# Optimization experiments

Hardware: AMD Instinct MI355X
Metric: run time of the kernel (lower is better)

## Reference

```python
import jax, jax.numpy as jnp
import numpy as np

N_SCALES = 3
BASE_SIGMA = 0.1
SCALES = jnp.asarray([BASE_SIGMA * 2.0 ** i for i in range(N_SCALES)], dtype=jnp.float32)


def setup_inputs() -> dict:
    key = jax.random.key(0)
    k_x, k_pos, k_tp, k_w1, k_b1, k_w2, k_b2 = jax.random.split(key, 7)
    B, C, T = 16, 306, 4000
    M = 128
    x = jax.random.normal(k_x, (B, C, T), dtype=jnp.float32)
    positions = jax.random.normal(k_pos, (B, C, 2), dtype=jnp.float32)
    target_positions = jax.random.normal(k_tp, (M, 2), dtype=jnp.float32)
    # nn.Linear(3, 32) / nn.Linear(32, 1) params (kaiming-uniform-ish init)
    lim1 = 1.0 / np.sqrt(3.0)
    w1 = jax.random.uniform(k_w1, (3, 32), jnp.float32, -lim1, lim1)
    b1 = jax.random.uniform(k_b1, (32,), jnp.float32, -lim1, lim1)
    lim2 = 1.0 / np.sqrt(32.0)
    w2 = jax.random.uniform(k_w2, (32, 1), jnp.float32, -lim2, lim2)
    b2 = jax.random.uniform(k_b2, (1,), jnp.float32, -lim2, lim2)
    return {"x": x, "positions": positions, "target_positions": target_positions,
            "w1": w1, "b1": b1, "w2": w2, "b2": b2}


def reference(x, positions, target_positions, w1, b1, w2, b2):
    # squared euclidean distances [B, C, M]
    diff = positions[:, :, None, :] - target_positions[None, None, :, :]
    d2 = jnp.sum(diff * diff, axis=-1)
    # multi-scale Gaussian kernels, stacked on last axis -> [B, C, M, n_scales]
    inv = 1.0 / (2.0 * SCALES ** 2)  # [n_scales]
    scale_weights = jnp.exp(-d2[..., None] * inv)
    # tiny 2-layer MLP gate: (3 -> 32 -> 1)
    h = jax.nn.relu(scale_weights @ w1 + b1)  # [B, C, M, 32]
    w = (h @ w2 + b2)[..., 0]                 # [B, C, M]
    # normalize over channel dim
    w = w / (jnp.sum(w, axis=1, keepdims=True) + 1e-8)
    # weighted channel aggregation -> [B, M, T]
    return jnp.einsum('bct,bcm->bmt', x, w)
```

## Files before the change

kernel.cpp:

```cpp
#include <hip/hip_runtime.h>

#define B_ 16
#define C_ 306
#define CP_ 320
#define T_ 4000
#define M_ 128

typedef short bf16x8 __attribute__((ext_vector_type(8)));
typedef float f32x4 __attribute__((ext_vector_type(4)));

__global__ __launch_bounds__(320)
void gate_kernel(const float* __restrict__ positions,
                 const float* __restrict__ target,
                 const float* __restrict__ w1,
                 const float* __restrict__ b1,
                 const float* __restrict__ w2,
                 const float* __restrict__ b2,
                 unsigned short* __restrict__ w_hi,
                 unsigned short* __restrict__ w_lo,
                 float* __restrict__ scale) {
    const int b  = blockIdx.x >> 5;
    const int mg = blockIdx.x & 31;
    const int tid = threadIdx.x;

    __shared__ float s_w1[96], s_b1[32], s_w2[32];
    __shared__ float2 s_pos[C_];
    __shared__ float s_b2;
    __shared__ float s_tgt[8];
    __shared__ float s_part[5];

    if (tid < 96) s_w1[tid] = w1[tid];
    if (tid < 32) { s_b1[tid] = b1[tid]; s_w2[tid] = w2[tid]; }
    if (tid == 256) s_b2 = b2[0];
    if (tid < C_) s_pos[tid] = ((const float2*)positions)[b * C_ + tid];
    if (tid >= 312) s_tgt[tid - 312] = target[mg * 8 + (tid - 312)];
    __syncthreads();

    float px = 0.0f, py = 0.0f;
    if (tid < C_) { px = s_pos[tid].x; py = s_pos[tid].y; }

#pragma unroll
    for (int mi = 0; mi < 4; ++mi) {
        float w = 0.0f;
        if (tid < C_) {
            const float dx = px - s_tgt[mi * 2 + 0];
            const float dy = py - s_tgt[mi * 2 + 1];
            const float d2 = dx * dx + dy * dy;
            const float s2 = __expf(-d2 * 3.125f);
            const float q  = s2 * s2;
            const float s1 = q * q;
            const float r  = s1 * s1;
            const float s0 = r * r;
            float acc = s_b2;
#pragma unroll
            for (int j = 0; j < 32; ++j) {
                float h = fmaf(s0, s_w1[j],
                          fmaf(s1, s_w1[32 + j],
                          fmaf(s2, s_w1[64 + j], s_b1[j])));
                acc = fmaf(fmaxf(h, 0.0f), s_w2[j], acc);
            }
            w = acc;
        }

        float s = w;
#pragma unroll
        for (int off = 32; off > 0; off >>= 1) s += __shfl_down(s, off, 64);
        if ((tid & 63) == 0) s_part[tid >> 6] = s;
        __syncthreads();
        if (tid == 0) {
            float tot = s_part[0] + s_part[1] + s_part[2] + s_part[3] + s_part[4];
            scale[b * M_ + mg * 4 + mi] = 1.0f / (tot + 1e-8f);
        }
        __syncthreads();

        const unsigned int u = __float_as_uint(w);
        const unsigned short h = (unsigned short)(u >> 16);
        const float lof = w - __uint_as_float(u & 0xffff0000u);
        const unsigned short l = (unsigned short)(__float_as_uint(lof) >> 16);
        const size_t off = (size_t)(b * M_ + mg * 4 + mi) * CP_ + tid;
        w_hi[off] = h;
        w_lo[off] = l;
    }
}

__global__ __launch_bounds__(256, 3)
void merge_gemm(const float* __restrict__ x,
                const unsigned short* __restrict__ w_hi,
                const unsigned short* __restrict__ w_lo,
                const float* __restrict__ scale,
                float* __restrict__ out) {
    const int t0 = blockIdx.x * 128;
    const int b  = blockIdx.y;
    const int tid  = threadIdx.x;
    const int lane = tid & 63;
    const int wv   = tid >> 6;
    const int tquad = lane >> 4;
    const int tsub  = lane & 15;

    __shared__ __align__(16) unsigned short sXh[8192];
    __shared__ __align__(16) unsigned short sXl[8192];
    __shared__ __align__(16) float sScale[M_];

    if (tid < M_) sScale[tid] = scale[b * M_ + tid];

    const float* xb = x + (size_t)b * C_ * T_;
    const unsigned short* whB = w_hi + (size_t)b * M_ * CP_;
    const unsigned short* wlB = w_lo + (size_t)b * M_ * CP_;

    f32x4 acc[4][4];
#pragma unroll
    for (int i = 0; i < 4; ++i)
#pragma unroll
        for (int j = 0; j < 4; ++j) acc[i][j] = (f32x4){0.f, 0.f, 0.f, 0.f};

    const int mw = (wv & 1) * 64;
    const int tw = (wv >> 1) * 64;

    for (int step = 0; step < CP_ / 64; ++step) {
        const int c0 = step * 64;

#pragma unroll
        for (int s = 0; s < 2; ++s) {
            const int t = wv * 16 + tsub + s * 64;
            const int tg = min(t0 + t, T_ - 1);
            const float* xcol = xb + tg;
#pragma unroll
            for (int k = 0; k < 8; ++k) {
                const int p = tquad + 4 * k;
                const int c = c0 + 2 * p;
                const int ca = min(c, C_ - 1);
                const int cb = min(c + 1, C_ - 1);
                const float xa = xcol[(size_t)ca * T_];
                const float xv = xcol[(size_t)cb * T_];
                const unsigned int ua = __float_as_uint(xa);
                const unsigned int ub = __float_as_uint(xv);
                const unsigned int hp = (ua >> 16) | (ub & 0xffff0000u);
                const float la = xa - __uint_as_float(ua & 0xffff0000u);
                const float lb = xv - __uint_as_float(ub & 0xffff0000u);
                const unsigned int lp = (__float_as_uint(la) >> 16) |
                                        (__float_as_uint(lb) & 0xffff0000u);
                const int off32 = (p >> 2) * 512 + t * 4 + (p & 3);
                ((unsigned int*)sXh)[off32] = hp;
                ((unsigned int*)sXl)[off32] = lp;
            }
        }
        __syncthreads();

#pragma unroll
        for (int ks = 0; ks < 2; ++ks) {
            const int cb0 = c0 + ks * 32;

            bf16x8 bh[4], bl[4];
#pragma unroll
            for (int i = 0; i < 4; ++i) {
                const int toff = ((ks * 4 + tquad) * 128 + tw + i * 16 + tsub) * 8;
                bh[i] = *(const bf16x8*)(sXh + toff);
                bl[i] = *(const bf16x8*)(sXl + toff);
            }
#pragma unroll
            for (int mi = 0; mi < 4; ++mi) {
                const size_t woff = (size_t)(mw + mi * 16 + tsub) * CP_ + cb0 + tquad * 8;
                const bf16x8 ah = *(const bf16x8*)(whB + woff);
                const bf16x8 al = *(const bf16x8*)(wlB + woff);
#pragma unroll
                for (int ti = 0; ti < 4; ++ti) {
                    acc[mi][ti] = __builtin_amdgcn_mfma_f32_16x16x32_bf16(
                        ah, bh[ti], acc[mi][ti], 0, 0, 0);
                    acc[mi][ti] = __builtin_amdgcn_mfma_f32_16x16x32_bf16(
                        ah, bl[ti], acc[mi][ti], 0, 0, 0);
                    acc[mi][ti] = __builtin_amdgcn_mfma_f32_16x16x32_bf16(
                        al, bh[ti], acc[mi][ti], 0, 0, 0);
                }
            }
        }
        __syncthreads();
    }

#pragma unroll
    for (int mi = 0; mi < 4; ++mi) {
        const int mbase = mw + mi * 16 + tquad * 4;
        const float4 sc = *(const float4*)(sScale + mbase);
#pragma unroll
        for (int ti = 0; ti < 4; ++ti) {
            const int tg = t0 + tw + ti * 16 + tsub;
            if (tg < T_) {
                float* op = out + ((size_t)b * M_ + mbase) * T_ + tg;
                op[0 * T_] = acc[mi][ti][0] * sc.x;
                op[1 * T_] = acc[mi][ti][1] * sc.y;
                op[2 * T_] = acc[mi][ti][2] * sc.z;
                op[3 * T_] = acc[mi][ti][3] * sc.w;
            }
        }
    }
}

extern "C" void kernel_launch(void* const* d_in, const int* in_sizes, int n_in,
                              void* d_out, int out_size, void* d_ws, size_t ws_size,
                              hipStream_t stream) {
    const float* x         = (const float*)d_in[0];
    const float* positions = (const float*)d_in[1];
    const float* target    = (const float*)d_in[2];
    const float* w1        = (const float*)d_in[3];
    const float* b1        = (const float*)d_in[4];
    const float* w2        = (const float*)d_in[5];
    const float* b2        = (const float*)d_in[6];
    float* out = (float*)d_out;

    unsigned short* w_hi = (unsigned short*)d_ws;
    unsigned short* w_lo = w_hi + (size_t)B_ * M_ * CP_;
    float* scale = (float*)(w_lo + (size_t)B_ * M_ * CP_);

    gate_kernel<<<B_ * 32, 320, 0, stream>>>(positions, target, w1, b1, w2, b2,
                                             w_hi, w_lo, scale);

    dim3 grid((T_ + 127) / 128, B_);
    merge_gemm<<<grid, 256, 0, stream>>>(x, w_hi, w_lo, scale, out);
}
```

Baseline: 151.4 us.

## Shrink GEMM tiles to 64x64, add M split, vectorize and prefetch x loads

The merge GEMM now uses 64(M)x64(T) tiles with a grid that also splits M, which gives more blocks for better CU occupancy. The x tile is loaded as float4 along T into registers and prefetched one step ahead, so the global load latency overlaps with the MFMA work. The padded LDS layout is meant to reduce bank conflicts. The trade-off is that x is now read twice, once per M half, and the smaller tiles give less reuse per block.

```diff
diff --git a/kernel.cpp b/kernel.cpp
--- a/kernel.cpp
+++ b/kernel.cpp
@@ -83,87 +83,110 @@
     }
 }
 
-__global__ __launch_bounds__(256, 3)
+__global__ __launch_bounds__(256, 4)
 void merge_gemm(const float* __restrict__ x,
                 const unsigned short* __restrict__ w_hi,
                 const unsigned short* __restrict__ w_lo,
                 const float* __restrict__ scale,
                 float* __restrict__ out) {
-    const int t0 = blockIdx.x * 128;
-    const int b  = blockIdx.y;
+    const int t0 = blockIdx.x * 64;
+    const int m0 = blockIdx.y * 64;
+    const int b  = blockIdx.z;
     const int tid  = threadIdx.x;
     const int lane = tid & 63;
     const int wv   = tid >> 6;
     const int tquad = lane >> 4;
     const int tsub  = lane & 15;
 
-    __shared__ __align__(16) unsigned short sXh[8192];
-    __shared__ __align__(16) unsigned short sXl[8192];
-    __shared__ __align__(16) float sScale[M_];
-
-    if (tid < M_) sScale[tid] = scale[b * M_ + tid];
+    __shared__ __align__(16) unsigned int sXh[2076];
+    __shared__ __align__(16) unsigned int sXl[2076];
+    __shared__ __align__(16) float sScale[64];
+
+    if (tid < 64) sScale[tid] = scale[b * M_ + m0 + tid];
 
     const float* xb = x + (size_t)b * C_ * T_;
-    const unsigned short* whB = w_hi + (size_t)b * M_ * CP_;
-    const unsigned short* wlB = w_lo + (size_t)b * M_ * CP_;
-
-    f32x4 acc[4][4];
-#pragma unroll
-    for (int i = 0; i < 4; ++i)
-#pragma unroll
-        for (int j = 0; j < 4; ++j) acc[i][j] = (f32x4){0.f, 0.f, 0.f, 0.f};
-
-    const int mw = (wv & 1) * 64;
-    const int tw = (wv >> 1) * 64;
-
-    for (int step = 0; step < CP_ / 64; ++step) {
-        const int c0 = step * 64;
-
-#pragma unroll
-        for (int s = 0; s < 2; ++s) {
-            const int t = wv * 16 + tsub + s * 64;
-            const int tg = min(t0 + t, T_ - 1);
-            const float* xcol = xb + tg;
-#pragma unroll
-            for (int k = 0; k < 8; ++k) {
-                const int p = tquad + 4 * k;
-                const int c = c0 + 2 * p;
-                const int ca = min(c, C_ - 1);
-                const int cb = min(c + 1, C_ - 1);
-                const float xa = xcol[(size_t)ca * T_];
-                const float xv = xcol[(size_t)cb * T_];
-                const unsigned int ua = __float_as_uint(xa);
-                const unsigned int ub = __float_as_uint(xv);
-                const unsigned int hp = (ua >> 16) | (ub & 0xffff0000u);
-                const float la = xa - __uint_as_float(ua & 0xffff0000u);
-                const float lb = xv - __uint_as_float(ub & 0xffff0000u);
-                const unsigned int lp = (__float_as_uint(la) >> 16) |
-                                        (__float_as_uint(lb) & 0xffff0000u);
-                const int off32 = (p >> 2) * 512 + t * 4 + (p & 3);
-                ((unsigned int*)sXh)[off32] = hp;
-                ((unsigned int*)sXl)[off32] = lp;
-            }
-        }
-        __syncthreads();
-
+    const unsigned short* whB = w_hi + (size_t)(b * M_ + m0) * CP_;
+    const unsigned short* wlB = w_lo + (size_t)(b * M_ + m0) * CP_;
+
+    const int mw = (wv & 1) * 32;
+    const int tw = (wv >> 1) * 32;
+
+    const int pp   = tid >> 4;
+    const int tq   = tid & 15;
+    const int runw = pp >> 1;
+    const int w0   = (pp & 1) * 2;
+    const float* xcol = xb + min(t0 + tq * 4, T_ - 4);
+
+    f32x4 acc[2][2];
+#pragma unroll
+    for (int i = 0; i < 2; ++i)
+#pragma unroll
+        for (int j = 0; j < 2; ++j) acc[i][j] = (f32x4){0.f, 0.f, 0.f, 0.f};
+
+    float4 rv[4];
+#pragma unroll
+    for (int r = 0; r < 4; ++r) {
+        const int c = min(pp * 4 + r, C_ - 1);
+        rv[r] = *(const float4*)(xcol + (size_t)c * T_);
+    }
+
+    for (int step = 0; step < 5; ++step) {
+        __syncthreads();
+        {
+            const float* f0 = (const float*)&rv[0];
+            const float* f1 = (const float*)&rv[1];
+            const float* f2 = (const float*)&rv[2];
+            const float* f3 = (const float*)&rv[3];
+            const int base = runw * 260 + tq * 16 + w0;
+#pragma unroll
+            for (int j = 0; j < 4; ++j) {
+                const unsigned int u0 = __float_as_uint(f0[j]);
+                const unsigned int u1 = __float_as_uint(f1[j]);
+                const unsigned int u2 = __float_as_uint(f2[j]);
+                const unsigned int u3 = __float_as_uint(f3[j]);
+                const unsigned int h01 = (u0 >> 16) | (u1 & 0xffff0000u);
+                const unsigned int h23 = (u2 >> 16) | (u3 & 0xffff0000u);
+                const float l0 = f0[j] - __uint_as_float(u0 & 0xffff0000u);
+                const float l1 = f1[j] - __uint_as_float(u1 & 0xffff0000u);
+                const float l2 = f2[j] - __uint_as_float(u2 & 0xffff0000u);
+                const float l3 = f3[j] - __uint_as_float(u3 & 0xffff0000u);
+                const unsigned int l01 = (__float_as_uint(l0) >> 16) |
+                                         (__float_as_uint(l1) & 0xffff0000u);
+                const unsigned int l23 = (__float_as_uint(l2) >> 16) |
+                                         (__float_as_uint(l3) & 0xffff0000u);
+                *(uint2*)(sXh + base + j * 4) = make_uint2(h01, h23);
+                *(uint2*)(sXl + base + j * 4) = make_uint2(l01, l23);
+            }
+        }
+        __syncthreads();
+
+        if (step < 4) {
+            const int c0n = (step + 1) * 64;
+#pragma unroll
+            for (int r = 0; r < 4; ++r) {
+                const int c = min(c0n + pp * 4 + r, C_ - 1);
+                rv[r] = *(const float4*)(xcol + (size_t)c * T_);
+            }
+        }
+
+        const int cbase = step * 64;
 #pragma unroll
         for (int ks = 0; ks < 2; ++ks) {
-            const int cb0 = c0 + ks * 32;
-
-            bf16x8 bh[4], bl[4];
-#pragma unroll
-            for (int i = 0; i < 4; ++i) {
-                const int toff = ((ks * 4 + tquad) * 128 + tw + i * 16 + tsub) * 8;
-                bh[i] = *(const bf16x8*)(sXh + toff);
-                bl[i] = *(const bf16x8*)(sXl + toff);
-            }
-#pragma unroll
-            for (int mi = 0; mi < 4; ++mi) {
-                const size_t woff = (size_t)(mw + mi * 16 + tsub) * CP_ + cb0 + tquad * 8;
+            bf16x8 bh[2], bl[2];
+#pragma unroll
+            for (int i = 0; i < 2; ++i) {
+                const int a = (ks * 4 + tquad) * 260 + (tw + i * 16 + tsub) * 4;
+                bh[i] = *(const bf16x8*)(sXh + a);
+                bl[i] = *(const bf16x8*)(sXl + a);
+            }
+#pragma unroll
+            for (int mi = 0; mi < 2; ++mi) {
+                const size_t woff = (size_t)(mw + mi * 16 + tsub) * CP_
+                                  + cbase + ks * 32 + tquad * 8;
                 const bf16x8 ah = *(const bf16x8*)(whB + woff);
                 const bf16x8 al = *(const bf16x8*)(wlB + woff);
 #pragma unroll
-                for (int ti = 0; ti < 4; ++ti) {
+                for (int ti = 0; ti < 2; ++ti) {
                     acc[mi][ti] = __builtin_amdgcn_mfma_f32_16x16x32_bf16(
                         ah, bh[ti], acc[mi][ti], 0, 0, 0);
                     acc[mi][ti] = __builtin_amdgcn_mfma_f32_16x16x32_bf16(
@@ -173,22 +196,21 @@
                 }
             }
         }
-        __syncthreads();
-    }
-
-#pragma unroll
-    for (int mi = 0; mi < 4; ++mi) {
-        const int mbase = mw + mi * 16 + tquad * 4;
-        const float4 sc = *(const float4*)(sScale + mbase);
-#pragma unroll
-        for (int ti = 0; ti < 4; ++ti) {
+    }
+
+#pragma unroll
+    for (int mi = 0; mi < 2; ++mi) {
+        const int mloc = mw + mi * 16 + tquad * 4;
+        const float4 sc = *(const float4*)(sScale + mloc);
+        float* op = out + ((size_t)b * M_ + m0 + mloc) * T_;
+#pragma unroll
+        for (int ti = 0; ti < 2; ++ti) {
             const int tg = t0 + tw + ti * 16 + tsub;
             if (tg < T_) {
-                float* op = out + ((size_t)b * M_ + mbase) * T_ + tg;
-                op[0 * T_] = acc[mi][ti][0] * sc.x;
-                op[1 * T_] = acc[mi][ti][1] * sc.y;
-                op[2 * T_] = acc[mi][ti][2] * sc.z;
-                op[3 * T_] = acc[mi][ti][3] * sc.w;
+                op[(size_t)0 * T_ + tg] = acc[mi][ti][0] * sc.x;
+                op[(size_t)1 * T_ + tg] = acc[mi][ti][1] * sc.y;
+                op[(size_t)2 * T_ + tg] = acc[mi][ti][2] * sc.z;
+                op[(size_t)3 * T_ + tg] = acc[mi][ti][3] * sc.w;
             }
         }
     }
@@ -213,6 +235,6 @@
     gate_kernel<<<B_ * 32, 320, 0, stream>>>(positions, target, w1, b1, w2, b2,
                                              w_hi, w_lo, scale);
 
-    dim3 grid((T_ + 127) / 128, B_);
+    dim3 grid((T_ + 63) / 64, 2, B_);
     merge_gemm<<<grid, 256, 0, stream>>>(x, w_hi, w_lo, scale, out);
 }
```

Measured after the change: 174.2 us. 1.15x slower.

## Vectorize x loads with register prefetch and fragment-ordered gate weights

Applied to the files above, without the earlier changes.

The GEMM now loads x as float4 along T into registers one K-step ahead, so global loads overlap the MFMA work, and writes them into a padded LDS layout that avoids bank conflicts. The gate kernel stages its hi/lo bf16 weights in shared memory and writes them to global memory in MFMA-fragment order, interleaving hi and lo, so the GEMM reads each A fragment pair contiguously. This removes the scalar strided x loads and the separate scattered hi/lo weight reads, at the cost of more registers for the prefetch buffers and a more complex indexing scheme.

```diff
diff --git a/kernel.cpp b/kernel.cpp
--- a/kernel.cpp
+++ b/kernel.cpp
@@ -8,6 +8,8 @@
 
 typedef short bf16x8 __attribute__((ext_vector_type(8)));
 typedef float f32x4 __attribute__((ext_vector_type(4)));
+
+#define WF_PER_B 81920
 
 __global__ __launch_bounds__(320)
 void gate_kernel(const float* __restrict__ positions,
@@ -16,8 +18,7 @@
                  const float* __restrict__ b1,
                  const float* __restrict__ w2,
                  const float* __restrict__ b2,
-                 unsigned short* __restrict__ w_hi,
-                 unsigned short* __restrict__ w_lo,
+                 unsigned short* __restrict__ wf,
                  float* __restrict__ scale) {
     const int b  = blockIdx.x >> 5;
     const int mg = blockIdx.x & 31;
@@ -28,6 +29,7 @@
     __shared__ float s_b2;
     __shared__ float s_tgt[8];
     __shared__ float s_part[5];
+    __shared__ unsigned short s_frag[40 * 72];
 
     if (tid < 96) s_w1[tid] = w1[tid];
     if (tid < 32) { s_b1[tid] = b1[tid]; s_w2[tid] = w2[tid]; }
@@ -38,6 +40,9 @@
 
     float px = 0.0f, py = 0.0f;
     if (tid < C_) { px = s_pos[tid].x; py = s_pos[tid].y; }
+
+    const int chunk = tid >> 3;
+    const int slot  = tid & 7;
 
 #pragma unroll
     for (int mi = 0; mi < 4; ++mi) {
@@ -77,16 +82,24 @@
         const unsigned short h = (unsigned short)(u >> 16);
         const float lof = w - __uint_as_float(u & 0xffff0000u);
         const unsigned short l = (unsigned short)(__float_as_uint(lof) >> 16);
-        const size_t off = (size_t)(b * M_ + mg * 4 + mi) * CP_ + tid;
-        w_hi[off] = h;
-        w_lo[off] = l;
+        s_frag[chunk * 72 + mi * 16 + 0 + slot] = h;
+        s_frag[chunk * 72 + mi * 16 + 8 + slot] = l;
+    }
+    __syncthreads();
+
+    {
+        const int ch = tid >> 3;
+        const int g  = tid & 7;
+        const uint4 v = *(const uint4*)(s_frag + ch * 72 + g * 8);
+        unsigned short* dst = wf + (size_t)b * WF_PER_B
+                            + (size_t)ch * 2048 + mg * 64 + g * 8;
+        *(uint4*)dst = v;
     }
 }
 
 __global__ __launch_bounds__(256, 3)
 void merge_gemm(const float* __restrict__ x,
-                const unsigned short* __restrict__ w_hi,
-                const unsigned short* __restrict__ w_lo,
+                const unsigned short* __restrict__ wf,
                 const float* __restrict__ scale,
                 float* __restrict__ out) {
     const int t0 = blockIdx.x * 128;
@@ -97,15 +110,14 @@
     const int tquad = lane >> 4;
     const int tsub  = lane & 15;
 
-    __shared__ __align__(16) unsigned short sXh[8192];
-    __shared__ __align__(16) unsigned short sXl[8192];
+    __shared__ __align__(16) unsigned int sXh[5120];
+    __shared__ __align__(16) unsigned int sXl[5120];
     __shared__ __align__(16) float sScale[M_];
 
     if (tid < M_) sScale[tid] = scale[b * M_ + tid];
 
     const float* xb = x + (size_t)b * C_ * T_;
-    const unsigned short* whB = w_hi + (size_t)b * M_ * CP_;
-    const unsigned short* wlB = w_lo + (size_t)b * M_ * CP_;
+    const unsigned short* wfB = wf + (size_t)b * WF_PER_B;
 
     f32x4 acc[4][4];
 #pragma unroll
@@ -116,52 +128,89 @@
     const int mw = (wv & 1) * 64;
     const int tw = (wv >> 1) * 64;
 
-    for (int step = 0; step < CP_ / 64; ++step) {
-        const int c0 = step * 64;
+    const int p  = tid >> 4;
+    const int tq = tid & 15;
+
+    float4 rv[8];
+#pragma unroll
+    for (int s = 0; s < 2; ++s) {
+        const int TQ  = tq + 16 * s;
+        const int tcl = min(t0 + TQ * 4, T_ - 4);
+#pragma unroll
+        for (int sub = 0; sub < 2; ++sub) {
+            const int cp = p + 16 * sub;
+            const int c  = 2 * cp;
+            rv[(s * 2 + sub) * 2 + 0] =
+                *(const float4*)(xb + (size_t)min(c, C_ - 1) * T_ + tcl);
+            rv[(s * 2 + sub) * 2 + 1] =
+                *(const float4*)(xb + (size_t)min(c + 1, C_ - 1) * T_ + tcl);
+        }
+    }
+
+    for (int step = 0; step < 5; ++step) {
+        __syncthreads();
 
 #pragma unroll
         for (int s = 0; s < 2; ++s) {
-            const int t = wv * 16 + tsub + s * 64;
-            const int tg = min(t0 + t, T_ - 1);
-            const float* xcol = xb + tg;
-#pragma unroll
-            for (int k = 0; k < 8; ++k) {
-                const int p = tquad + 4 * k;
-                const int c = c0 + 2 * p;
-                const int ca = min(c, C_ - 1);
-                const int cb = min(c + 1, C_ - 1);
-                const float xa = xcol[(size_t)ca * T_];
-                const float xv = xcol[(size_t)cb * T_];
-                const unsigned int ua = __float_as_uint(xa);
-                const unsigned int ub = __float_as_uint(xv);
-                const unsigned int hp = (ua >> 16) | (ub & 0xffff0000u);
-                const float la = xa - __uint_as_float(ua & 0xffff0000u);
-                const float lb = xv - __uint_as_float(ub & 0xffff0000u);
-                const unsigned int lp = (__float_as_uint(la) >> 16) |
-                                        (__float_as_uint(lb) & 0xffff0000u);
-                const int off32 = (p >> 2) * 512 + t * 4 + (p & 3);
-                ((unsigned int*)sXh)[off32] = hp;
-                ((unsigned int*)sXl)[off32] = lp;
-            }
-        }
-        __syncthreads();
+            const int TQ = tq + 16 * s;
+#pragma unroll
+            for (int sub = 0; sub < 2; ++sub) {
+                const int cp  = p + 16 * sub;
+                const int run = cp >> 2;
+                const int pw  = cp & 3;
+                const float* fa = (const float*)&rv[(s * 2 + sub) * 2 + 0];
+                const float* fb = (const float*)&rv[(s * 2 + sub) * 2 + 1];
+                const int base = run * 640 + TQ * 20 + pw;
+#pragma unroll
+                for (int tt = 0; tt < 4; ++tt) {
+                    const unsigned int ua = __float_as_uint(fa[tt]);
+                    const unsigned int ub = __float_as_uint(fb[tt]);
+                    const float la = fa[tt] - __uint_as_float(ua & 0xffff0000u);
+                    const float lb = fb[tt] - __uint_as_float(ub & 0xffff0000u);
+                    sXh[base + tt * 4] = (ua >> 16) | (ub & 0xffff0000u);
+                    sXl[base + tt * 4] = (__float_as_uint(la) >> 16) |
+                                         (__float_as_uint(lb) & 0xffff0000u);
+                }
+            }
+        }
+        __syncthreads();
+
+        if (step < 4) {
+            const int c0n = (step + 1) * 64;
+#pragma unroll
+            for (int s = 0; s < 2; ++s) {
+                const int TQ  = tq + 16 * s;
+                const int tcl = min(t0 + TQ * 4, T_ - 4);
+#pragma unroll
+                for (int sub = 0; sub < 2; ++sub) {
+                    const int c = c0n + 2 * (p + 16 * sub);
+                    rv[(s * 2 + sub) * 2 + 0] =
+                        *(const float4*)(xb + (size_t)min(c, C_ - 1) * T_ + tcl);
+                    rv[(s * 2 + sub) * 2 + 1] =
+                        *(const float4*)(xb + (size_t)min(c + 1, C_ - 1) * T_ + tcl);
+                }
+            }
+        }
 
 #pragma unroll
         for (int ks = 0; ks < 2; ++ks) {
-            const int cb0 = c0 + ks * 32;
+            const int sub64 = step * 2 + ks;
+            const int runb  = ks * 4 + tquad;
 
             bf16x8 bh[4], bl[4];
 #pragma unroll
             for (int i = 0; i < 4; ++i) {
-                const int toff = ((ks * 4 + tquad) * 128 + tw + i * 16 + tsub) * 8;
-                bh[i] = *(const bf16x8*)(sXh + toff);
-                bl[i] = *(const bf16x8*)(sXl + toff);
+                const int t = tw + i * 16 + tsub;
+                const int a = runb * 640 + (t >> 2) * 20 + (t & 3) * 4;
+                bh[i] = *(const bf16x8*)(sXh + a);
+                bl[i] = *(const bf16x8*)(sXl + a);
             }
 #pragma unroll
             for (int mi = 0; mi < 4; ++mi) {
-                const size_t woff = (size_t)(mw + mi * 16 + tsub) * CP_ + cb0 + tquad * 8;
-                const bf16x8 ah = *(const bf16x8*)(whB + woff);
-                const bf16x8 al = *(const bf16x8*)(wlB + woff);
+                const size_t aoff = ((size_t)(sub64 * 4 + tquad) * 128
+                                   + (mw + mi * 16 + tsub)) * 16;
+                const bf16x8 ah = *(const bf16x8*)(wfB + aoff);
+                const bf16x8 al = *(const bf16x8*)(wfB + aoff + 8);
 #pragma unroll
                 for (int ti = 0; ti < 4; ++ti) {
                     acc[mi][ti] = __builtin_amdgcn_mfma_f32_16x16x32_bf16(
@@ -173,22 +222,21 @@
                 }
             }
         }
-        __syncthreads();
     }
 
 #pragma unroll
     for (int mi = 0; mi < 4; ++mi) {
         const int mbase = mw + mi * 16 + tquad * 4;
         const float4 sc = *(const float4*)(sScale + mbase);
+        float* op = out + ((size_t)b * M_ + mbase) * T_;
 #pragma unroll
         for (int ti = 0; ti < 4; ++ti) {
             const int tg = t0 + tw + ti * 16 + tsub;
             if (tg < T_) {
-                float* op = out + ((size_t)b * M_ + mbase) * T_ + tg;
-                op[0 * T_] = acc[mi][ti][0] * sc.x;
-                op[1 * T_] = acc[mi][ti][1] * sc.y;
-                op[2 * T_] = acc[mi][ti][2] * sc.z;
-                op[3 * T_] = acc[mi][ti][3] * sc.w;
+                op[(size_t)0 * T_ + tg] = acc[mi][ti][0] * sc.x;
+                op[(size_t)1 * T_ + tg] = acc[mi][ti][1] * sc.y;
+                op[(size_t)2 * T_ + tg] = acc[mi][ti][2] * sc.z;
+                op[(size_t)3 * T_ + tg] = acc[mi][ti][3] * sc.w;
             }
         }
     }
@@ -206,13 +254,12 @@
     const float* b2        = (const float*)d_in[6];
     float* out = (float*)d_out;
 
-    unsigned short* w_hi = (unsigned short*)d_ws;
-    unsigned short* w_lo = w_hi + (size_t)B_ * M_ * CP_;
-    float* scale = (float*)(w_lo + (size_t)B_ * M_ * CP_);
+    float* scale = (float*)d_ws;
+    unsigned short* wf = (unsigned short*)(scale + B_ * M_);
 
     gate_kernel<<<B_ * 32, 320, 0, stream>>>(positions, target, w1, b1, w2, b2,
-                                             w_hi, w_lo, scale);
+                                             wf, scale);
 
     dim3 grid((T_ + 127) / 128, B_);
-    merge_gemm<<<grid, 256, 0, stream>>>(x, w_hi, w_lo, scale, out);
+    merge_gemm<<<grid, 256, 0, stream>>>(x, wf, scale, out);
 }
```

Result: no change. 150.5 us (-0.6%).
